# Optimization experiments

Measured on AMD Instinct MI355X. Metric: run time of the kernel, lower is better.

## Reference

```python
import jax, jax.numpy as jnp
import numpy as np

B, S, HID, NH = 8, 1024, 1024, 16
DH = HID // NH
ZERO = 1e-8  # undefined repo constant, assumed small epsilon


def setup_inputs() -> dict:
    key = jax.random.key(0)
    ks = jax.random.split(key, 14)
    sc = 1.0 / np.sqrt(HID)
    inp = {
        "Q": jax.random.normal(ks[0], (B, S, HID), jnp.float32),
        "K": jax.random.normal(ks[1], (B, S, HID), jnp.float32),
        "V": jax.random.normal(ks[2], (B, S, HID), jnp.float32),
        "Q_mask": jax.random.randint(ks[3], (B, S), 0, 2).astype(jnp.float32),
        "K_mask": jax.random.randint(ks[4], (B, S), 0, 2).astype(jnp.float32),
        "Wq": jax.random.normal(ks[5], (HID, HID), jnp.float32) * sc,
        "bq": jnp.zeros((HID,), jnp.float32),
        "Wk": jax.random.normal(ks[6], (HID, HID), jnp.float32) * sc,
        "bk": jnp.zeros((HID,), jnp.float32),
        "Wv": jax.random.normal(ks[7], (HID, HID), jnp.float32) * sc,
        "bv": jnp.zeros((HID,), jnp.float32),
        "Wo": jax.random.normal(ks[8], (HID, HID), jnp.float32) * sc,
        "bo": jnp.zeros((HID,), jnp.float32),
    }
    return inp


def _heads(x):  # [B,S,HID] -> [B,NH,S,DH]
    b, s, _ = x.shape
    return x.reshape(b, s, NH, DH).transpose(0, 2, 1, 3)


def reference(Q, K, V, Q_mask, K_mask, Wq, bq, Wk, bk, Wv, bv, Wo, bo):
    q = _heads(Q @ Wq.T + bq)
    k = _heads(K @ Wk.T + bk)
    v = _heads(V @ Wv.T + bv)
    # NOTE: original divides by head_size**(-0.5) == multiply by sqrt(DH)
    scores = jnp.einsum("bhqd,bhkd->bhqk", q, k) / (DH ** (-0.5))
    mask = Q_mask[:, :, None] * K_mask[:, None, :]  # [B,Sq,Sk]
    probs = jax.nn.softmax(scores, axis=-1)
    probs = jnp.where(mask[:, None, :, :] == 0, 0.0, probs)
    probs = probs / jnp.sum(probs + ZERO, axis=-1, keepdims=True)
    ctx = jnp.einsum("bhqk,bhkd->bqhd", probs, v).reshape(Q.shape[0], Q.shape[1], HID)
    return ctx @ Wo.T + bo
```

## Files before the change

### kernel.cpp

```cpp
#include <hip/hip_runtime.h>
#include <math.h>

constexpr int Bc   = 8;
constexpr int Sc   = 1024;
constexpr int HIDc = 1024;
constexpr int NHc  = 16;
constexpr int DHc  = 64;
constexpr int Mc   = Bc * Sc;
constexpr int Kc2  = 1024;
constexpr float SCALE    = 8.0f;
constexpr float EPS_TERM = 1024.0f * 1e-8f;

typedef short s16x8 __attribute__((ext_vector_type(8)));
typedef float f32x4 __attribute__((ext_vector_type(4)));

__device__ __forceinline__ ushort f2bf(float f) {
  unsigned u = __float_as_uint(f);
  u += 0x7FFFu + ((u >> 16) & 1u);
  return (ushort)(u >> 16);
}
__device__ __forceinline__ float bf2f(ushort h) {
  return __uint_as_float(((unsigned)h) << 16);
}

__device__ __forceinline__ void gl_lds16(const ushort* g, ushort* l) {
  __builtin_amdgcn_global_load_lds(
      (const __attribute__((address_space(1))) void*)g,
      (__attribute__((address_space(3))) void*)l, 16, 0, 0);
}

__global__ __launch_bounds__(256) void cvt_split(const float4* __restrict__ x,
    ushort4* __restrict__ hi, ushort4* __restrict__ lo, int n4)
{
  const int i = blockIdx.x * 256 + threadIdx.x;
  if (i >= n4) return;
  const float4 v = x[i];
  ushort4 h, l;
  h.x = f2bf(v.x); l.x = f2bf(v.x - bf2f(h.x));
  h.y = f2bf(v.y); l.y = f2bf(v.y - bf2f(h.y));
  h.z = f2bf(v.z); l.z = f2bf(v.z - bf2f(h.z));
  h.w = f2bf(v.w); l.w = f2bf(v.w - bf2f(h.w));
  hi[i] = h; lo[i] = l;
}

__global__ __launch_bounds__(256) void cvt_one(const float4* __restrict__ x,
    ushort4* __restrict__ hi, int n4)
{
  const int i = blockIdx.x * 256 + threadIdx.x;
  if (i >= n4) return;
  const float4 v = x[i];
  ushort4 h;
  h.x = f2bf(v.x); h.y = f2bf(v.y); h.z = f2bf(v.z); h.w = f2bf(v.w);
  hi[i] = h;
}

__global__ __launch_bounds__(256) void cvt_weights(
    const float4* __restrict__ Wq, const float4* __restrict__ Wk,
    const float4* __restrict__ Wv, const float4* __restrict__ Wo,
    ushort4* __restrict__ Wqh, ushort4* __restrict__ Wql,
    ushort4* __restrict__ Wkh, ushort4* __restrict__ Wkl,
    ushort4* __restrict__ Wvh, ushort4* __restrict__ Woh, int n4w)
{
  const int bpseg = n4w / 256;
  const int seg   = blockIdx.x / bpseg;
  const int li    = (blockIdx.x - seg * bpseg) * 256 + threadIdx.x;
  if (li >= n4w) return;
  if (seg == 0) {
    const float4 v = Wq[li];
    ushort4 h, l;
    h.x = f2bf(v.x); l.x = f2bf(v.x - bf2f(h.x));
    h.y = f2bf(v.y); l.y = f2bf(v.y - bf2f(h.y));
    h.z = f2bf(v.z); l.z = f2bf(v.z - bf2f(h.z));
    h.w = f2bf(v.w); l.w = f2bf(v.w - bf2f(h.w));
    Wqh[li] = h; Wql[li] = l;
  } else if (seg == 1) {
    const float4 v = Wk[li];
    ushort4 h, l;
    h.x = f2bf(v.x); l.x = f2bf(v.x - bf2f(h.x));
    h.y = f2bf(v.y); l.y = f2bf(v.y - bf2f(h.y));
    h.z = f2bf(v.z); l.z = f2bf(v.z - bf2f(h.z));
    h.w = f2bf(v.w); l.w = f2bf(v.w - bf2f(h.w));
    Wkh[li] = h; Wkl[li] = l;
  } else {
    const float4 v = (seg == 2) ? Wv[li] : Wo[li];
    ushort4 h;
    h.x = f2bf(v.x); h.y = f2bf(v.y); h.z = f2bf(v.z); h.w = f2bf(v.w);
    if (seg == 2) Wvh[li] = h; else Woh[li] = h;
  }
}

template<bool SPLIT3>
__global__ __launch_bounds__(256, 3) void mfma_gemm(
    const ushort* __restrict__ Ah_g, const ushort* __restrict__ Al_g,
    const ushort* __restrict__ Bh_g, const ushort* __restrict__ Bl_g,
    const float* __restrict__ bias,
    void* __restrict__ C, void* __restrict__ C2, int mode)
{
  __shared__ ushort AhL[4096];
  __shared__ ushort BhL[4096];
  __shared__ ushort AlL[SPLIT3 ? 4096 : 8];
  __shared__ ushort BlL[SPLIT3 ? 4096 : 8];

  const int t    = threadIdx.x;
  const int w    = t >> 6;
  const int ln   = t & 63;
  const int col  = ln & 15;
  const int quad = ln >> 4;
  const int wm   = w >> 1, wn = w & 1;
  const int m0   = blockIdx.y * 128;
  const int n0   = blockIdx.x * 128;

  f32x4 acc[4][4] = {};

  const int sA = w * 128;

  for (int k0 = 0; k0 < Kc2; k0 += 32) {
    __syncthreads();
#pragma unroll
    for (int j = 0; j < 2; j++) {
      const int s = sA + j * 64 + ln;
      const int r = s & 127, c = s >> 7;
      const size_t goA = (size_t)(m0 + r) * Kc2 + k0 + c * 8;
      const size_t goB = (size_t)(n0 + r) * Kc2 + k0 + c * 8;
      ushort* la = &AhL[(size_t)(sA + j * 64) * 8];
      ushort* lb = &BhL[(size_t)(sA + j * 64) * 8];
      gl_lds16(Ah_g + goA, la);
      gl_lds16(Bh_g + goB, lb);
      if constexpr (SPLIT3) {
        gl_lds16(Al_g + goA, &AlL[(size_t)(sA + j * 64) * 8]);
        gl_lds16(Bl_g + goB, &BlL[(size_t)(sA + j * 64) * 8]);
      }
    }
    __syncthreads();

    s16x8 a_h[4], b_h[4], a_l[4], b_l[4];
#pragma unroll
    for (int i = 0; i < 4; i++) {
      const int ai = (quad * 128 + wm * 64 + i * 16 + col) * 8;
      const int bi = (quad * 128 + wn * 64 + i * 16 + col) * 8;
      a_h[i] = *(const s16x8*)&AhL[ai];
      b_h[i] = *(const s16x8*)&BhL[bi];
      if constexpr (SPLIT3) {
        a_l[i] = *(const s16x8*)&AlL[ai];
        b_l[i] = *(const s16x8*)&BlL[bi];
      }
    }
#pragma unroll
    for (int i = 0; i < 4; i++)
#pragma unroll
      for (int jj = 0; jj < 4; jj++) {
        acc[i][jj] = __builtin_amdgcn_mfma_f32_16x16x32_bf16(a_h[i], b_h[jj], acc[i][jj], 0, 0, 0);
        if constexpr (SPLIT3) {
          acc[i][jj] = __builtin_amdgcn_mfma_f32_16x16x32_bf16(a_h[i], b_l[jj], acc[i][jj], 0, 0, 0);
          acc[i][jj] = __builtin_amdgcn_mfma_f32_16x16x32_bf16(a_l[i], b_h[jj], acc[i][jj], 0, 0, 0);
        }
      }
  }

  const int mb = m0 + wm * 64;
  const int nb = n0 + wn * 64;
#pragma unroll
  for (int i = 0; i < 4; i++)
#pragma unroll
    for (int jj = 0; jj < 4; jj++) {
      const int n  = nb + jj * 16 + col;
      const float bv = bias[n];
#pragma unroll
      for (int r = 0; r < 4; r++) {
        const int m   = mb + i * 16 + quad * 4 + r;
        const float v = acc[i][jj][r] + bv;
        if (mode == 0) {
          ((float*)C)[(size_t)m * HIDc + n] = v;
        } else {
          const int b_ = m >> 10, s = m & (Sc - 1);
          const int h_ = n >> 6,  d = n & (DHc - 1);
          if (mode == 1) {
            const size_t off = (((size_t)b_ * NHc + h_) * Sc + s) * DHc + d;
            const ushort hb = f2bf(v);
            ((ushort*)C)[off]  = hb;
            ((ushort*)C2)[off] = f2bf(v - bf2f(hb));
          } else {
            const size_t off = (((size_t)b_ * NHc + h_) * DHc + d) * Sc + s;
            ((ushort*)C)[off] = f2bf(v);
          }
        }
      }
    }
}

constexpr int TK  = 64;
constexpr int LDK = 80;
constexpr int LDP = 72;

__global__ __launch_bounds__(256, 3) void attn_mfma(
    const ushort* __restrict__ qhi, const ushort* __restrict__ qlo,
    const ushort* __restrict__ khi, const ushort* __restrict__ klo,
    const ushort* __restrict__ vt,  const float* __restrict__ Qm,
    const float* __restrict__ Km,   ushort* __restrict__ ctx)
{
  __shared__ ushort KhiL[64 * LDK];
  __shared__ ushort KloL[64 * LDK];
  __shared__ ushort VtL [64 * LDK];
  __shared__ ushort PmL [64 * LDP];
  __shared__ float  kmL[TK];

  const int t    = threadIdx.x;
  const int w    = t >> 6;
  const int ln   = t & 63;
  const int col  = ln & 15;
  const int quad = ln >> 4;

  const int id  = blockIdx.x;
  const int xcd = id & 7;
  const int j   = id >> 3;
  const int bh  = xcd * 16 + (j >> 4);
  const int qt  = j & 15;
  const int b   = bh >> 4;
  const int h   = bh & 15;

  const int qbase = qt * 64 + w * 16;
  const size_t headoff = (size_t)bh * Sc * DHc;

  s16x8 qh0, qh1, ql0, ql1;
  {
    const size_t ro = headoff + (size_t)(qbase + col) * DHc + quad * 8;
    qh0 = *(const s16x8*)(qhi + ro);
    qh1 = *(const s16x8*)(qhi + ro + 32);
    ql0 = *(const s16x8*)(qlo + ro);
    ql1 = *(const s16x8*)(qlo + ro + 32);
  }

  f32x4 O[4] = {{0,0,0,0},{0,0,0,0},{0,0,0,0},{0,0,0,0}};
  float mrow[4] = {-INFINITY, -INFINITY, -INFINITY, -INFINITY};
  float Zr[4]   = {0,0,0,0};
  float Zmr[4]  = {0,0,0,0};

  for (int k0 = 0; k0 < Sc; k0 += TK) {
    __syncthreads();
    for (int i = t; i < 512; i += 256) {
      const int rr = i >> 3, cc = (i & 7) * 8;
      *(s16x8*)&KhiL[rr * LDK + cc] = *(const s16x8*)(khi + headoff + (size_t)(k0 + rr) * DHc + cc);
      *(s16x8*)&KloL[rr * LDK + cc] = *(const s16x8*)(klo + headoff + (size_t)(k0 + rr) * DHc + cc);
      *(s16x8*)&VtL [rr * LDK + cc] = *(const s16x8*)(vt  + headoff + (size_t)rr * Sc + k0 + cc);
    }
    if (t < TK) kmL[t] = Km[b * Sc + k0 + t];
    __syncthreads();

    float s[4][4];
#pragma unroll
    for (int ks = 0; ks < 4; ks++) {
      const ushort* kp = &KhiL[(ks * 16 + col) * LDK];
      const ushort* lp = &KloL[(ks * 16 + col) * LDK];
      const s16x8 kh0 = *(const s16x8*)(kp + quad * 8);
      const s16x8 kh1 = *(const s16x8*)(kp + 32 + quad * 8);
      const s16x8 kl0 = *(const s16x8*)(lp + quad * 8);
      const s16x8 kl1 = *(const s16x8*)(lp + 32 + quad * 8);
      f32x4 acc = {0,0,0,0};
      acc = __builtin_amdgcn_mfma_f32_16x16x32_bf16(qh0, kh0, acc, 0, 0, 0);
      acc = __builtin_amdgcn_mfma_f32_16x16x32_bf16(qh1, kh1, acc, 0, 0, 0);
      acc = __builtin_amdgcn_mfma_f32_16x16x32_bf16(qh0, kl0, acc, 0, 0, 0);
      acc = __builtin_amdgcn_mfma_f32_16x16x32_bf16(qh1, kl1, acc, 0, 0, 0);
      acc = __builtin_amdgcn_mfma_f32_16x16x32_bf16(ql0, kh0, acc, 0, 0, 0);
      acc = __builtin_amdgcn_mfma_f32_16x16x32_bf16(ql1, kh1, acc, 0, 0, 0);
#pragma unroll
      for (int r = 0; r < 4; r++) s[ks][r] = acc[r] * SCALE;
    }

    float kmv[4];
#pragma unroll
    for (int ks = 0; ks < 4; ks++) kmv[ks] = kmL[ks * 16 + col];

    float tmax[4];
#pragma unroll
    for (int r = 0; r < 4; r++)
      tmax[r] = fmaxf(fmaxf(s[0][r], s[1][r]), fmaxf(s[2][r], s[3][r]));
#pragma unroll
    for (int off = 1; off < 16; off <<= 1)
#pragma unroll
      for (int r = 0; r < 4; r++)
        tmax[r] = fmaxf(tmax[r], __shfl_xor(tmax[r], off, 64));

    float alpha[4];
#pragma unroll
    for (int r = 0; r < 4; r++) {
      const float mn = fmaxf(mrow[r], tmax[r]);
      alpha[r] = __expf(mrow[r] - mn);
      mrow[r]  = mn;
    }

#pragma unroll
    for (int r = 0; r < 4; r++) {
      float ps = 0.0f, pms = 0.0f;
#pragma unroll
      for (int ks = 0; ks < 4; ks++) {
        const float p  = __expf(s[ks][r] - mrow[r]);
        const float pm = p * kmv[ks];
        ps  += p;
        pms += pm;
        s[ks][r] = pm;
      }
      Zr[r]  = Zr[r]  * alpha[r] + ps;
      Zmr[r] = Zmr[r] * alpha[r] + pms;
    }

#pragma unroll
    for (int ks = 0; ks < 4; ks++)
#pragma unroll
      for (int r = 0; r < 4; r++)
        PmL[(w * 16 + quad * 4 + r) * LDP + ks * 16 + col] = f2bf(s[ks][r]);
#pragma unroll
    for (int dt = 0; dt < 4; dt++)
#pragma unroll
      for (int r = 0; r < 4; r++)
        O[dt][r] *= alpha[r];

    const ushort* pp = &PmL[(w * 16 + col) * LDP];
    const s16x8 p0 = *(const s16x8*)(pp + quad * 8);
    const s16x8 p1 = *(const s16x8*)(pp + 32 + quad * 8);
#pragma unroll
    for (int dt = 0; dt < 4; dt++) {
      const ushort* vp = &VtL[(dt * 16 + col) * LDK];
      const s16x8 v0 = *(const s16x8*)(vp + quad * 8);
      const s16x8 v1 = *(const s16x8*)(vp + 32 + quad * 8);
      O[dt] = __builtin_amdgcn_mfma_f32_16x16x32_bf16(p0, v0, O[dt], 0, 0, 0);
      O[dt] = __builtin_amdgcn_mfma_f32_16x16x32_bf16(p1, v1, O[dt], 0, 0, 0);
    }
  }

#pragma unroll
  for (int off = 1; off < 16; off <<= 1)
#pragma unroll
    for (int r = 0; r < 4; r++) {
      Zr[r]  += __shfl_xor(Zr[r],  off, 64);
      Zmr[r] += __shfl_xor(Zmr[r], off, 64);
    }

#pragma unroll
  for (int r = 0; r < 4; r++) {
    const int srow = qbase + quad * 4 + r;
    const float qmv  = Qm[b * Sc + srow];
    const float rden = (qmv != 0.0f) ? 1.0f / (Zmr[r] + EPS_TERM * Zr[r]) : 0.0f;
#pragma unroll
    for (int dt = 0; dt < 4; dt++)
      ctx[((size_t)(b * Sc + srow)) * HIDc + h * DHc + dt * 16 + col] = f2bf(O[dt][r] * rden);
  }
}

extern "C" void kernel_launch(void* const* d_in, const int* in_sizes, int n_in,
                              void* d_out, int out_size, void* d_ws, size_t ws_size,
                              hipStream_t stream)
{
  const float* Q  = (const float*)d_in[0];
  const float* K  = (const float*)d_in[1];
  const float* V  = (const float*)d_in[2];
  const float* Qm = (const float*)d_in[3];
  const float* Km = (const float*)d_in[4];
  const float* Wq = (const float*)d_in[5];
  const float* bq = (const float*)d_in[6];
  const float* Wk = (const float*)d_in[7];
  const float* bk = (const float*)d_in[8];
  const float* Wv = (const float*)d_in[9];
  const float* bv = (const float*)d_in[10];
  const float* Wo = (const float*)d_in[11];
  const float* bo = (const float*)d_in[12];
  float* out = (float*)d_out;

  const size_t NEL = (size_t)Mc * HIDc;
  const size_t WEL = (size_t)HIDc * HIDc;

  ushort* Wqh = (ushort*)d_ws;
  ushort* Wql = Wqh + WEL;
  ushort* Wkh = Wql + WEL;
  ushort* Wkl = Wkh + WEL;
  ushort* Wvh = Wkl + WEL;
  ushort* Woh = Wvh + WEL;
  ushort* qhi = Woh + WEL;
  ushort* qlo = qhi + NEL;
  ushort* khi = qlo + NEL;
  ushort* klo = khi + NEL;
  ushort* vt  = klo + NEL;
  ushort* A0  = vt  + NEL;
  ushort* A1  = A0  + NEL;

  const int n4i = (int)(NEL / 4);
  const int n4w = (int)(WEL / 4);

  cvt_weights<<<4 * (n4w / 256), 256, 0, stream>>>(
      (const float4*)Wq, (const float4*)Wk, (const float4*)Wv, (const float4*)Wo,
      (ushort4*)Wqh, (ushort4*)Wql, (ushort4*)Wkh, (ushort4*)Wkl,
      (ushort4*)Wvh, (ushort4*)Woh, n4w);

  dim3 gg(HIDc / 128, Mc / 128);

  cvt_split<<<n4i / 256, 256, 0, stream>>>((const float4*)Q, (ushort4*)A0, (ushort4*)A1, n4i);
  mfma_gemm<true><<<gg, 256, 0, stream>>>(A0, A1, Wqh, Wql, bq, qhi, qlo, 1);

  cvt_split<<<n4i / 256, 256, 0, stream>>>((const float4*)K, (ushort4*)A0, (ushort4*)A1, n4i);
  mfma_gemm<true><<<gg, 256, 0, stream>>>(A0, A1, Wkh, Wkl, bk, khi, klo, 1);

  cvt_one<<<n4i / 256, 256, 0, stream>>>((const float4*)V, (ushort4*)A0, n4i);
  mfma_gemm<false><<<gg, 256, 0, stream>>>(A0, nullptr, Wvh, nullptr, bv, vt, nullptr, 2);

  attn_mfma<<<Bc * NHc * (Sc / 64), 256, 0, stream>>>(qhi, qlo, khi, klo, vt, Qm, Km, A1);

  mfma_gemm<false><<<gg, 256, 0, stream>>>(A1, nullptr, Woh, nullptr, bo, out, nullptr, 0);
}
```

Measured before the change: 532.4 us.

## Transpose attention MFMA orientation and stage K/V via direct global-to-LDS loads

Swaps the MFMA operand order so each lane owns a single query row (S^T and O^T). This turns the per-row max and sum reductions into two cross-quad shuffles instead of four-step butterflies over four rows. K/V tiles are now loaded with global_load_lds into a chunked LDS layout, replacing register-staged copies. P and output stores are packed into uint2 writes, and the occupancy hint rises to 4 blocks per CU. The main risks are LDS bank conflicts from the new unpadded chunk layout and higher register pressure under the tighter launch bound.

```diff
diff --git a/kernel.cpp b/kernel.cpp
--- a/kernel.cpp
+++ b/kernel.cpp
@@ -21,6 +21,9 @@
 }
 __device__ __forceinline__ float bf2f(ushort h) {
   return __uint_as_float(((unsigned)h) << 16);
+}
+__device__ __forceinline__ unsigned pk2bf(float a, float b) {
+  return (unsigned)f2bf(a) | ((unsigned)f2bf(b) << 16);
 }
 
 __device__ __forceinline__ void gl_lds16(const ushort* g, ushort* l) {
@@ -188,21 +191,19 @@
     }
 }
 
-constexpr int TK  = 64;
-constexpr int LDK = 80;
 constexpr int LDP = 72;
 
-__global__ __launch_bounds__(256, 3) void attn_mfma(
+__global__ __launch_bounds__(256, 4) void attn_mfma(
     const ushort* __restrict__ qhi, const ushort* __restrict__ qlo,
     const ushort* __restrict__ khi, const ushort* __restrict__ klo,
     const ushort* __restrict__ vt,  const float* __restrict__ Qm,
     const float* __restrict__ Km,   ushort* __restrict__ ctx)
 {
-  __shared__ ushort KhiL[64 * LDK];
-  __shared__ ushort KloL[64 * LDK];
-  __shared__ ushort VtL [64 * LDK];
+  __shared__ ushort KhiL[4096];
+  __shared__ ushort KloL[4096];
+  __shared__ ushort VtL [4096];
   __shared__ ushort PmL [64 * LDP];
-  __shared__ float  kmL[TK];
+  __shared__ float  kmL[64];
 
   const int t    = threadIdx.x;
   const int w    = t >> 6;
@@ -230,119 +231,101 @@
     ql1 = *(const s16x8*)(qlo + ro + 32);
   }
 
-  f32x4 O[4] = {{0,0,0,0},{0,0,0,0},{0,0,0,0},{0,0,0,0}};
-  float mrow[4] = {-INFINITY, -INFINITY, -INFINITY, -INFINITY};
-  float Zr[4]   = {0,0,0,0};
-  float Zmr[4]  = {0,0,0,0};
-
-  for (int k0 = 0; k0 < Sc; k0 += TK) {
+  f32x4 OT[4] = {{0,0,0,0},{0,0,0,0},{0,0,0,0},{0,0,0,0}};
+  float mrow = -INFINITY;
+  float Zp = 0.0f, Zmp = 0.0f;
+
+  for (int k0 = 0; k0 < Sc; k0 += 64) {
     __syncthreads();
-    for (int i = t; i < 512; i += 256) {
-      const int rr = i >> 3, cc = (i & 7) * 8;
-      *(s16x8*)&KhiL[rr * LDK + cc] = *(const s16x8*)(khi + headoff + (size_t)(k0 + rr) * DHc + cc);
-      *(s16x8*)&KloL[rr * LDK + cc] = *(const s16x8*)(klo + headoff + (size_t)(k0 + rr) * DHc + cc);
-      *(s16x8*)&VtL [rr * LDK + cc] = *(const s16x8*)(vt  + headoff + (size_t)rr * Sc + k0 + cc);
-    }
-    if (t < TK) kmL[t] = Km[b * Sc + k0 + t];
+#pragma unroll
+    for (int jj = 0; jj < 2; jj++) {
+      const int c = jj * 4 + w;
+      const size_t gk = headoff + (size_t)(k0 + ln) * DHc + c * 8;
+      const size_t gv = headoff + (size_t)ln * Sc + k0 + c * 8;
+      gl_lds16(khi + gk, &KhiL[c * 512]);
+      gl_lds16(klo + gk, &KloL[c * 512]);
+      gl_lds16(vt  + gv, &VtL [c * 512]);
+    }
+    if (t < 64) kmL[t] = Km[b * Sc + k0 + t];
     __syncthreads();
 
     float s[4][4];
 #pragma unroll
     for (int ks = 0; ks < 4; ks++) {
-      const ushort* kp = &KhiL[(ks * 16 + col) * LDK];
-      const ushort* lp = &KloL[(ks * 16 + col) * LDK];
-      const s16x8 kh0 = *(const s16x8*)(kp + quad * 8);
-      const s16x8 kh1 = *(const s16x8*)(kp + 32 + quad * 8);
-      const s16x8 kl0 = *(const s16x8*)(lp + quad * 8);
-      const s16x8 kl1 = *(const s16x8*)(lp + 32 + quad * 8);
-      f32x4 acc = {0,0,0,0};
-      acc = __builtin_amdgcn_mfma_f32_16x16x32_bf16(qh0, kh0, acc, 0, 0, 0);
-      acc = __builtin_amdgcn_mfma_f32_16x16x32_bf16(qh1, kh1, acc, 0, 0, 0);
-      acc = __builtin_amdgcn_mfma_f32_16x16x32_bf16(qh0, kl0, acc, 0, 0, 0);
-      acc = __builtin_amdgcn_mfma_f32_16x16x32_bf16(qh1, kl1, acc, 0, 0, 0);
-      acc = __builtin_amdgcn_mfma_f32_16x16x32_bf16(ql0, kh0, acc, 0, 0, 0);
-      acc = __builtin_amdgcn_mfma_f32_16x16x32_bf16(ql1, kh1, acc, 0, 0, 0);
-#pragma unroll
-      for (int r = 0; r < 4; r++) s[ks][r] = acc[r] * SCALE;
-    }
-
-    float kmv[4];
-#pragma unroll
-    for (int ks = 0; ks < 4; ks++) kmv[ks] = kmL[ks * 16 + col];
-
-    float tmax[4];
-#pragma unroll
-    for (int r = 0; r < 4; r++)
-      tmax[r] = fmaxf(fmaxf(s[0][r], s[1][r]), fmaxf(s[2][r], s[3][r]));
-#pragma unroll
-    for (int off = 1; off < 16; off <<= 1)
-#pragma unroll
-      for (int r = 0; r < 4; r++)
-        tmax[r] = fmaxf(tmax[r], __shfl_xor(tmax[r], off, 64));
-
-    float alpha[4];
-#pragma unroll
-    for (int r = 0; r < 4; r++) {
-      const float mn = fmaxf(mrow[r], tmax[r]);
-      alpha[r] = __expf(mrow[r] - mn);
-      mrow[r]  = mn;
-    }
-
-#pragma unroll
-    for (int r = 0; r < 4; r++) {
-      float ps = 0.0f, pms = 0.0f;
-#pragma unroll
-      for (int ks = 0; ks < 4; ks++) {
-        const float p  = __expf(s[ks][r] - mrow[r]);
-        const float pm = p * kmv[ks];
-        ps  += p;
-        pms += pm;
-        s[ks][r] = pm;
-      }
-      Zr[r]  = Zr[r]  * alpha[r] + ps;
-      Zmr[r] = Zmr[r] * alpha[r] + pms;
-    }
-
+      const int base0 = (quad * 64 + ks * 16 + col) * 8;
+      const int base1 = ((quad + 4) * 64 + ks * 16 + col) * 8;
+      const s16x8 kh0 = *(const s16x8*)&KhiL[base0];
+      const s16x8 kh1 = *(const s16x8*)&KhiL[base1];
+      const s16x8 kl0 = *(const s16x8*)&KloL[base0];
+      const s16x8 kl1 = *(const s16x8*)&KloL[base1];
+      f32x4 a = {0,0,0,0};
+      a = __builtin_amdgcn_mfma_f32_16x16x32_bf16(kh0, qh0, a, 0, 0, 0);
+      a = __builtin_amdgcn_mfma_f32_16x16x32_bf16(kh1, qh1, a, 0, 0, 0);
+      a = __builtin_amdgcn_mfma_f32_16x16x32_bf16(kh0, ql0, a, 0, 0, 0);
+      a = __builtin_amdgcn_mfma_f32_16x16x32_bf16(kh1, ql1, a, 0, 0, 0);
+      a = __builtin_amdgcn_mfma_f32_16x16x32_bf16(kl0, qh0, a, 0, 0, 0);
+      a = __builtin_amdgcn_mfma_f32_16x16x32_bf16(kl1, qh1, a, 0, 0, 0);
+#pragma unroll
+      for (int r = 0; r < 4; r++) s[ks][r] = a[r] * SCALE;
+    }
+
+    float tmax = s[0][0];
 #pragma unroll
     for (int ks = 0; ks < 4; ks++)
 #pragma unroll
-      for (int r = 0; r < 4; r++)
-        PmL[(w * 16 + quad * 4 + r) * LDP + ks * 16 + col] = f2bf(s[ks][r]);
-#pragma unroll
-    for (int dt = 0; dt < 4; dt++)
-#pragma unroll
-      for (int r = 0; r < 4; r++)
-        O[dt][r] *= alpha[r];
-
-    const ushort* pp = &PmL[(w * 16 + col) * LDP];
-    const s16x8 p0 = *(const s16x8*)(pp + quad * 8);
-    const s16x8 p1 = *(const s16x8*)(pp + 32 + quad * 8);
+      for (int r = 0; r < 4; r++) tmax = fmaxf(tmax, s[ks][r]);
+    tmax = fmaxf(tmax, __shfl_xor(tmax, 16, 64));
+    tmax = fmaxf(tmax, __shfl_xor(tmax, 32, 64));
+
+    const float mn    = fmaxf(mrow, tmax);
+    const float alpha = __expf(mrow - mn);
+    mrow = mn;
+
+    float ps = 0.0f, pms = 0.0f;
+    const int prow = (w * 16 + col) * LDP;
+#pragma unroll
+    for (int ks = 0; ks < 4; ks++) {
+      const float4 km4 = *(const float4*)&kmL[ks * 16 + quad * 4];
+      const float p0 = __expf(s[ks][0] - mn), p1 = __expf(s[ks][1] - mn);
+      const float p2 = __expf(s[ks][2] - mn), p3 = __expf(s[ks][3] - mn);
+      const float q0 = p0 * km4.x, q1 = p1 * km4.y, q2 = p2 * km4.z, q3 = p3 * km4.w;
+      ps  += (p0 + p1) + (p2 + p3);
+      pms += (q0 + q1) + (q2 + q3);
+      uint2 pv;
+      pv.x = pk2bf(q0, q1);
+      pv.y = pk2bf(q2, q3);
+      *(uint2*)&PmL[prow + ks * 16 + quad * 4] = pv;
+    }
+    Zp  = Zp  * alpha + ps;
+    Zmp = Zmp * alpha + pms;
+#pragma unroll
+    for (int dt = 0; dt < 4; dt++) OT[dt] *= alpha;
+
+    const s16x8 p0 = *(const s16x8*)&PmL[prow + quad * 8];
+    const s16x8 p1 = *(const s16x8*)&PmL[prow + 32 + quad * 8];
 #pragma unroll
     for (int dt = 0; dt < 4; dt++) {
-      const ushort* vp = &VtL[(dt * 16 + col) * LDK];
-      const s16x8 v0 = *(const s16x8*)(vp + quad * 8);
-      const s16x8 v1 = *(const s16x8*)(vp + 32 + quad * 8);
-      O[dt] = __builtin_amdgcn_mfma_f32_16x16x32_bf16(p0, v0, O[dt], 0, 0, 0);
-      O[dt] = __builtin_amdgcn_mfma_f32_16x16x32_bf16(p1, v1, O[dt], 0, 0, 0);
-    }
-  }
-
-#pragma unroll
-  for (int off = 1; off < 16; off <<= 1)
-#pragma unroll
-    for (int r = 0; r < 4; r++) {
-      Zr[r]  += __shfl_xor(Zr[r],  off, 64);
-      Zmr[r] += __shfl_xor(Zmr[r], off, 64);
-    }
-
-#pragma unroll
-  for (int r = 0; r < 4; r++) {
-    const int srow = qbase + quad * 4 + r;
-    const float qmv  = Qm[b * Sc + srow];
-    const float rden = (qmv != 0.0f) ? 1.0f / (Zmr[r] + EPS_TERM * Zr[r]) : 0.0f;
-#pragma unroll
-    for (int dt = 0; dt < 4; dt++)
-      ctx[((size_t)(b * Sc + srow)) * HIDc + h * DHc + dt * 16 + col] = f2bf(O[dt][r] * rden);
+      const s16x8 a0 = *(const s16x8*)&VtL[(quad * 64 + dt * 16 + col) * 8];
+      const s16x8 a1 = *(const s16x8*)&VtL[((quad + 4) * 64 + dt * 16 + col) * 8];
+      OT[dt] = __builtin_amdgcn_mfma_f32_16x16x32_bf16(a0, p0, OT[dt], 0, 0, 0);
+      OT[dt] = __builtin_amdgcn_mfma_f32_16x16x32_bf16(a1, p1, OT[dt], 0, 0, 0);
+    }
+  }
+
+  Zp  += __shfl_xor(Zp,  16, 64);  Zp  += __shfl_xor(Zp,  32, 64);
+  Zmp += __shfl_xor(Zmp, 16, 64);  Zmp += __shfl_xor(Zmp, 32, 64);
+
+  const int q     = qbase + col;
+  const float qmv = Qm[b * Sc + q];
+  const float rden = (qmv != 0.0f) ? 1.0f / (Zmp + EPS_TERM * Zp) : 0.0f;
+
+  ushort* crow = ctx + (size_t)(b * Sc + q) * HIDc + h * DHc + quad * 4;
+#pragma unroll
+  for (int dt = 0; dt < 4; dt++) {
+    uint2 ov;
+    ov.x = pk2bf(OT[dt][0] * rden, OT[dt][1] * rden);
+    ov.y = pk2bf(OT[dt][2] * rden, OT[dt][3] * rden);
+    *(uint2*)(crow + dt * 16) = ov;
   }
 }
 
```

After: 531.5 us. Within noise of the previous version (-0.2%).
